# Kernel optimization log

Hardware: AMD Instinct MI355X
Metric: run time of the kernel (lower is better)

The kernel has to match this reference:

```python
import jax, jax.numpy as jnp
import numpy as np

N = 50000
E = 800000
NODE_DIM = 128
EDGE_DIM = 32
HIDDEN = 128


def _linear_params(key, fan_in, fan_out):
    kw, kb = jax.random.split(key)
    bound = 1.0 / np.sqrt(fan_in)
    W = jax.random.uniform(kw, (fan_in, fan_out), minval=-bound, maxval=bound, dtype=jnp.float32)
    b = jax.random.uniform(kb, (fan_out,), minval=-bound, maxval=bound, dtype=jnp.float32)
    return W, b


def setup_inputs() -> dict:
    key = jax.random.key(0)
    ks = jax.random.split(key, 7)
    h = jax.random.normal(ks[0], (N, NODE_DIM), dtype=jnp.float32)
    edge_index = jax.random.randint(ks[1], (2, E), 0, N, dtype=jnp.int64)
    edge_attr = jax.random.normal(ks[2], (E, EDGE_DIM), dtype=jnp.float32)
    # message_fn: Linear(2*node+edge -> hidden), ReLU, Linear(hidden -> hidden), ReLU
    Wm1, bm1 = _linear_params(ks[3], 2 * NODE_DIM + EDGE_DIM, HIDDEN)
    Wm2, bm2 = _linear_params(ks[4], HIDDEN, HIDDEN)
    # update_fn: Linear(node+hidden -> hidden), ReLU, Linear(hidden -> node)
    Wu1, bu1 = _linear_params(ks[5], NODE_DIM + HIDDEN, HIDDEN)
    Wu2, bu2 = _linear_params(ks[6], HIDDEN, NODE_DIM)
    return {"h": h, "edge_attr": edge_attr, "Wm1": Wm1, "bm1": bm1, "Wm2": Wm2, "bm2": bm2,
            "Wu1": Wu1, "bu1": bu1, "Wu2": Wu2, "bu2": bu2, "edge_index": edge_index}


def reference(h, edge_attr, Wm1, bm1, Wm2, bm2, Wu1, bu1, Wu2, bu2, edge_index):
    src = edge_index[0]
    dst = edge_index[1]
    # m_ij = phi_m(h_i, h_j, e_ij)
    msg_input = jnp.concatenate([h[src], h[dst], edge_attr], axis=-1)  # (E, 2*node+edge)
    x = jax.nn.relu(msg_input @ Wm1 + bm1)
    messages = jax.nn.relu(x @ Wm2 + bm2)  # (E, hidden)
    # scatter-add over destination nodes
    agg = jax.ops.segment_sum(messages, dst, num_segments=N)  # (N, hidden)
    # h_i' = h_i + phi_u(h_i, agg_i)
    update_input = jnp.concatenate([h, agg], axis=-1)
    u = jax.nn.relu(update_input @ Wu1 + bu1)
    h_new = h + (u @ Wu2 + bu2)
    return h_new
```

## Files before the change

### kernel.cpp

```cpp
#include <hip/hip_runtime.h>

#define NN 50000
#define NE 800000

typedef __attribute__((ext_vector_type(8))) short bf16x8;
typedef __attribute__((ext_vector_type(4))) float f32x4;

__device__ __forceinline__ short f2bf(float f) {
    union { float f; unsigned u; } v; v.f = f;
    return (short)((v.u + 0x7fffu + ((v.u >> 16) & 1u)) >> 16);
}

__device__ __forceinline__ float bf2f(short s) {
    union { unsigned u; float f; } v;
    v.u = ((unsigned)(unsigned short)s) << 16;
    return v.f;
}

__device__ __forceinline__ bf16x8 cvt8(const float* __restrict__ p) {
    const f32x4 a = *(const f32x4*)p;
    const f32x4 b = *(const f32x4*)(p + 4);
    bf16x8 r;
#pragma unroll
    for (int j = 0; j < 4; ++j) { r[j] = f2bf(a[j]); r[j + 4] = f2bf(b[j]); }
    return r;
}

__device__ __forceinline__ void gld_lds16(const short* g, short* l) {
    __builtin_amdgcn_global_load_lds(
        (const __attribute__((address_space(1))) void*)g,
        (__attribute__((address_space(3))) void*)l, 16, 0, 0);
}

#define GW_M1A 0
#define GW_M1B 16384
#define GW_1C  32768
#define GW_M2S 36864
#define GW_U1A 53248
#define GW_U1B 69632
#define GW_U2S 86016
#define GW_TOT 102400

template<int KROWS, int NTHREADS>
__device__ __forceinline__ void stage_w(const float* __restrict__ W, short* lds, int tid) {
    constexpr int NSLOT = (KROWS / 32) * 8 * 64;
#pragma unroll 1
    for (int slot = tid; slot < NSLOT; slot += NTHREADS) {
        const int f = slot >> 6, l = slot & 63;
        const int s = f >> 3, t = f & 7;
        const int k0 = 32 * s + ((l >> 4) << 3);
        const int n = 16 * t + (l & 15);
        bf16x8 v;
#pragma unroll
        for (int j = 0; j < 8; ++j) v[j] = f2bf(W[(k0 + j) * 128 + n]);
        *(bf16x8*)(lds + slot * 8) = v;
    }
}

template<int NSLOT, int NTHREADS>
__device__ __forceinline__ void stage_copy(const short* __restrict__ g, short* lds, int tid) {
#pragma unroll 1
    for (int s = tid; s < NSLOT; s += NTHREADS) {
        *(bf16x8*)(lds + (size_t)s * 8) = *(const bf16x8*)(g + (size_t)s * 8);
    }
}


__global__ __launch_bounds__(256) void mega_kernel(
    const float* __restrict__ h, const float* __restrict__ Wm1,
    const float* __restrict__ bm1, const float* __restrict__ Wm2,
    const float* __restrict__ Wu1, const float* __restrict__ Wu2,
    const int* __restrict__ eidx, short* __restrict__ gW,
    short* __restrict__ Pb, short* __restrict__ Qb, int* __restrict__ cnt)
{
    const int b = blockIdx.x;
    const int tid = threadIdx.x;
    if (b < 512) {
        __shared__ short sWa[16384];
        __shared__ short sWb[16384];
        stage_w<128, 256>(Wm1, sWa, tid);
        stage_w<128, 256>(Wm1 + 128 * 128, sWb, tid);
        __syncthreads();
        const int wave = tid >> 6, lane = tid & 63;
        const int q = lane >> 4, col = lane & 15;
        float b1v[8];
#pragma unroll
        for (int t = 0; t < 8; ++t) b1v[t] = bm1[t * 16 + col];
        for (int tile = b * 4 + wave; tile < NN / 16; tile += 2048) {
            const int r0 = tile * 16;
            f32x4 aP[8], aQ[8];
#pragma unroll
            for (int t = 0; t < 8; ++t) {
                aP[t] = {0.f, 0.f, 0.f, 0.f};
                const float bb = b1v[t];
                aQ[t] = {bb, bb, bb, bb};
            }
#pragma unroll
            for (int s = 0; s < 4; ++s) {
                const bf16x8 ah = cvt8(&h[(r0 + col) * 128 + s * 32 + q * 8]);
#pragma unroll
                for (int t = 0; t < 8; ++t) {
                    const bf16x8 ba = *(const bf16x8*)(sWa + ((s * 8 + t) * 64 + lane) * 8);
                    const bf16x8 bb = *(const bf16x8*)(sWb + ((s * 8 + t) * 64 + lane) * 8);
                    aP[t] = __builtin_amdgcn_mfma_f32_16x16x32_bf16(ah, ba, aP[t], 0, 0, 0);
                    aQ[t] = __builtin_amdgcn_mfma_f32_16x16x32_bf16(ah, bb, aQ[t], 0, 0, 0);
                }
            }
#pragma unroll
            for (int r = 0; r < 4; ++r) {
                const size_t row = (size_t)(r0 + q * 4 + r) * 128;
                bf16x8 vp, vq;
#pragma unroll
                for (int t = 0; t < 8; ++t) { vp[t] = f2bf(aP[t][r]); vq[t] = f2bf(aQ[t][r]); }
                *(bf16x8*)(Pb + row + col * 8) = vp;
                *(bf16x8*)(Qb + row + col * 8) = vq;
            }
        }
    } else if (b < 562) {
        const int slot = (b - 512) * 256 + tid;
        if (slot < 12800) {
            const float* W; int local; bool sigma = false;
            if (slot < 2048)       { W = Wm1;             local = slot; }
            else if (slot < 4096)  { W = Wm1 + 128 * 128; local = slot - 2048; }
            else if (slot < 4608)  { W = Wm1 + 256 * 128; local = slot - 4096; }
            else if (slot < 6656)  { W = Wm2;             local = slot - 4608; sigma = true; }
            else if (slot < 8704)  { W = Wu1;             local = slot - 6656; }
            else if (slot < 10752) { W = Wu1 + 128 * 128; local = slot - 8704; }
            else                   { W = Wu2;             local = slot - 10752; sigma = true; }
            const int f = local >> 6, l = local & 63;
            const int s = f >> 3, t = f & 7;
            const int k0 = 32 * s + ((l >> 4) << 3);
            const int n = 16 * t + (l & 15);
            bf16x8 v;
#pragma unroll
            for (int j = 0; j < 8; ++j) {
                int k = k0 + j;
                if (sigma) k = (k & 7) * 16 + (k >> 3);
                v[j] = f2bf(W[k * 128 + n]);
            }
            *(bf16x8*)(gW + (size_t)slot * 8) = v;
        }
    } else {
        const int e = (b - 562) * 256 + tid;
        if (e < NE) atomicAdd(&cnt[eidx[NE + e]], 1);
    }
}


__global__ __launch_bounds__(1024) void scan1_kernel(const int* __restrict__ cnt,
                                                     int* __restrict__ part,
                                                     int* __restrict__ bsum) {
    __shared__ int s[1024];
    const int t = threadIdx.x;
    const int i = blockIdx.x * 1024 + t;
    const int v = (i < NN) ? cnt[i] : 0;
    int x = v;
    s[t] = x;
    __syncthreads();
    for (int off = 1; off < 1024; off <<= 1) {
        const int y = (t >= off) ? s[t - off] : 0;
        __syncthreads();
        x += y;
        s[t] = x;
        __syncthreads();
    }
    if (i < NN) part[i] = x - v;
    if (t == 1023) bsum[blockIdx.x] = x;
}

__global__ __launch_bounds__(1024) void scan23_kernel(const int* __restrict__ part,
                                                      const int* __restrict__ bsum,
                                                      int* __restrict__ cursor) {
    __shared__ int off;
    if (threadIdx.x == 0) {
        int a = 0;
        for (int bb = 0; bb < (int)blockIdx.x; ++bb) a += bsum[bb];
        off = a;
    }
    __syncthreads();
    const int i = blockIdx.x * 1024 + threadIdx.x;
    if (i < NN) cursor[i] = part[i] + off;
}


__global__ void scatter_kernel(const int* __restrict__ eidx, int* __restrict__ cursor,
                               const float* __restrict__ ea,
                               int2* __restrict__ sd2, short* __restrict__ eb) {
    const int e = blockIdx.x * blockDim.x + threadIdx.x;
    if (e < NE) {
        const int d = eidx[NE + e];
        const int pos = atomicAdd(&cursor[d], 1);
        sd2[pos] = make_int2(eidx[e], d);
        const float* src = ea + (size_t)e * 32;
        short* dst = eb + (size_t)pos * 32;
#pragma unroll
        for (int j = 0; j < 4; ++j) {
            const f32x4 a = *(const f32x4*)(src + j * 8);
            const f32x4 bq = *(const f32x4*)(src + j * 8 + 4);
            bf16x8 v;
#pragma unroll
            for (int k = 0; k < 4; ++k) { v[k] = f2bf(a[k]); v[4 + k] = f2bf(bq[k]); }
            *(bf16x8*)(dst + j * 8) = v;
        }
    }
}

#define WPB 7
#define TPW 28

__global__ __launch_bounds__(448, 2) void edge_kernel(
    const short* __restrict__ Pb, const short* __restrict__ Qb,
    const short* __restrict__ eb, const short* __restrict__ gW,
    const float* __restrict__ bm2,
    const int2* __restrict__ sd2, float* __restrict__ agg)
{
    __shared__ short sW2[16384];
    __shared__ short sW1c[4096];
    __shared__ short sPool[WPB][2][4096];
    const int tid = threadIdx.x;
    const int wave = tid >> 6, lane = tid & 63;
    const int q = lane >> 4, col = lane & 15;
    const int NT = NE / 16;
    float b2v[8];
#pragma unroll
    for (int t = 0; t < 8; ++t) b2v[t] = bm2[t * 16 + col];
    stage_copy<2048, 448>(gW + GW_M2S, sW2, tid);
    stage_copy<512, 448>(gW + GW_1C, sW1c, tid);

    const int wg = blockIdx.x * WPB + wave;
    const int t_begin = wg * TPW;
    const int t_end = (t_begin + TPW < NT) ? (t_begin + TPW) : NT;
    const bool act = t_begin < t_end;

    short* bufc = &sPool[wave][0][0];
    short* bufa = &sPool[wave][1][0];
    int2 sd_c[4], sd_n[4];
    bf16x8 aea_c;

    if (act) {
        {
            const int e0 = t_begin * 16;
            const int4 a0 = *(const int4*)(sd2 + e0 + q * 4);
            const int4 a1 = *(const int4*)(sd2 + e0 + q * 4 + 2);
            sd_c[0] = make_int2(a0.x, a0.y); sd_c[1] = make_int2(a0.z, a0.w);
            sd_c[2] = make_int2(a1.x, a1.y); sd_c[3] = make_int2(a1.z, a1.w);
        }
#pragma unroll
        for (int r = 0; r < 4; ++r) {
            gld_lds16(Pb + (size_t)sd_c[r].x * 128 + col * 8, bufc + r * 512);
            gld_lds16(Qb + (size_t)sd_c[r].y * 128 + col * 8, bufc + 2048 + r * 512);
        }
        {
            const int t1 = (t_begin + 1 < t_end) ? t_begin + 1 : t_begin;
            const int e1 = t1 * 16;
            const int4 a0 = *(const int4*)(sd2 + e1 + q * 4);
            const int4 a1 = *(const int4*)(sd2 + e1 + q * 4 + 2);
            sd_n[0] = make_int2(a0.x, a0.y); sd_n[1] = make_int2(a0.z, a0.w);
            sd_n[2] = make_int2(a1.x, a1.y); sd_n[3] = make_int2(a1.z, a1.w);
        }
        aea_c = *(const bf16x8*)(eb + (size_t)(t_begin * 16 + col) * 32 + q * 8);
    }
    __syncthreads();

    for (int tile = t_begin; tile < t_end; ++tile) {
        const int tn = (tile + 1 < t_end) ? tile + 1 : tile;
        asm volatile("s_waitcnt vmcnt(0)" ::: "memory");
        bf16x8 vp[4], vq[4];
#pragma unroll
        for (int r = 0; r < 4; ++r) {
            vp[r] = *(const bf16x8*)(bufc + r * 512 + lane * 8);
            vq[r] = *(const bf16x8*)(bufc + 2048 + r * 512 + lane * 8);
        }
#pragma unroll
        for (int r = 0; r < 4; ++r) {
            gld_lds16(Pb + (size_t)sd_n[r].x * 128 + col * 8, bufa + r * 512);
            gld_lds16(Qb + (size_t)sd_n[r].y * 128 + col * 8, bufa + 2048 + r * 512);
        }
        const bf16x8 aea_n = *(const bf16x8*)(eb + (size_t)(tn * 16 + col) * 32 + q * 8);
        int2 sd_n2[4];
        {
            const int t2 = (tile + 2 < t_end) ? tile + 2 : t_end - 1;
            const int e2 = t2 * 16;
            const int4 a0 = *(const int4*)(sd2 + e2 + q * 4);
            const int4 a1 = *(const int4*)(sd2 + e2 + q * 4 + 2);
            sd_n2[0] = make_int2(a0.x, a0.y); sd_n2[1] = make_int2(a0.z, a0.w);
            sd_n2[2] = make_int2(a1.x, a1.y); sd_n2[3] = make_int2(a1.z, a1.w);
        }
        const int prev3 = __shfl_up(sd_c[3].y, 16);
        unsigned qm = 0;
        if (q > 0 && sd_c[0].y == prev3) qm |= 1u;
        if (sd_c[1].y == sd_c[0].y) qm |= 2u;
        if (sd_c[2].y == sd_c[1].y) qm |= 4u;
        if (sd_c[3].y == sd_c[2].y) qm |= 8u;
        const unsigned o1 = (unsigned)__shfl_xor((int)qm, 16);
        const unsigned o2 = (unsigned)__shfl_xor((int)qm, 32);
        const unsigned o3 = (unsigned)__shfl_xor((int)o1, 32);
        const unsigned eqmask = (qm << (q * 4)) | (o1 << ((q ^ 1) * 4)) |
                                (o2 << ((q ^ 2) * 4)) | (o3 << ((q ^ 3) * 4));
        f32x4 acc1[8];
#pragma unroll
        for (int r = 0; r < 4; ++r) {
            const bf16x8 vpr = vp[r], vqr = vq[r];
#pragma unroll
            for (int t = 0; t < 8; ++t)
                acc1[t][r] = bf2f(vpr[t]) + bf2f(vqr[t]);
        }
#pragma unroll
        for (int t = 0; t < 8; ++t) {
            const bf16x8 bw = *(const bf16x8*)(sW1c + (t * 64 + lane) * 8);
            acc1[t] = __builtin_amdgcn_mfma_f32_16x16x32_bf16(aea_c, bw, acc1[t], 0, 0, 0);
        }
        short* myX = bufc;
#pragma unroll
        for (int r = 0; r < 4; ++r) {
            bf16x8 vx;
#pragma unroll
            for (int t = 0; t < 8; ++t) {
                const float x = acc1[t][r];
                vx[t] = f2bf(x > 0.f ? x : 0.f);
            }
            *(bf16x8*)(myX + (q * 4 + r) * 136 + col * 8) = vx;
        }
        f32x4 acc2[8];
#pragma unroll
        for (int t = 0; t < 8; ++t) {
            const float b = b2v[t];
            acc2[t] = {b, b, b, b};
        }
#pragma unroll
        for (int s = 0; s < 4; ++s) {
            const bf16x8 ax = *(const bf16x8*)(myX + col * 136 + s * 32 + q * 8);
#pragma unroll
            for (int t = 0; t < 8; ++t) {
                const bf16x8 bw = *(const bf16x8*)(sW2 + ((s * 8 + t) * 64 + lane) * 8);
                acc2[t] = __builtin_amdgcn_mfma_f32_16x16x32_bf16(ax, bw, acc2[t], 0, 0, 0);
            }
        }
        if (eqmask == 0xFFFEu) {
#pragma unroll
            for (int t = 0; t < 8; ++t) {
                float m0 = acc2[t][0]; m0 = m0 > 0.f ? m0 : 0.f;
                float m1 = acc2[t][1]; m1 = m1 > 0.f ? m1 : 0.f;
                float m2 = acc2[t][2]; m2 = m2 > 0.f ? m2 : 0.f;
                float m3 = acc2[t][3]; m3 = m3 > 0.f ? m3 : 0.f;
                float s = (m0 + m1) + (m2 + m3);
                s += __shfl_xor(s, 16);
                s += __shfl_xor(s, 32);
                if (q == 0 && s != 0.f)
                    unsafeAtomicAdd(&agg[(size_t)sd_c[0].y * 128 + t * 16 + col], s);
            }
        } else {
            int head[4], qe[4];
#pragma unroll
            for (int r = 0; r < 4; ++r) {
                const int e = q * 4 + r;
                head[r] = !((eqmask >> e) & 1u);
                const unsigned after = ~(eqmask >> (e + 1));
                const int run = __builtin_ctz(after);
                qe[r] = (e + run) >> 2;
            }
#pragma unroll
            for (int t = 0; t < 8; ++t) {
                float m0 = acc2[t][0]; m0 = m0 > 0.f ? m0 : 0.f;
                float m1 = acc2[t][1]; m1 = m1 > 0.f ? m1 : 0.f;
                float m2 = acc2[t][2]; m2 = m2 > 0.f ? m2 : 0.f;
                float m3 = acc2[t][3]; m3 = m3 > 0.f ? m3 : 0.f;
                const float s3 = m3;
                const float s2 = m2 + ((qm & 8u) ? s3 : 0.f);
                const float s1 = m1 + ((qm & 4u) ? s2 : 0.f);
                const float s0 = m0 + ((qm & 2u) ? s1 : 0.f);
                const float p1 = __shfl_xor(s0, 16);
                const float p2 = __shfl_xor(s0, 32);
                const float p3 = __shfl_xor(p1, 32);
                const float seg[4] = {s0, s1, s2, s3};
#pragma unroll
                for (int r = 0; r < 4; ++r) {
                    if (head[r]) {
                        float tot = seg[r];
#pragma unroll
                        for (int j = 1; j < 4; ++j) {
                            if (j > q && j <= qe[r]) {
                                const int jx = j ^ q;
                                tot += (jx == 1) ? p1 : (jx == 2) ? p2 : p3;
                            }
                        }
                        if (tot != 0.f)
                            unsafeAtomicAdd(&agg[(size_t)sd_c[r].y * 128 + t * 16 + col], tot);
                    }
                }
            }
        }
#pragma unroll
        for (int r = 0; r < 4; ++r) { sd_c[r] = sd_n[r]; sd_n[r] = sd_n2[r]; }
        aea_c = aea_n;
        short* tmp = bufc; bufc = bufa; bufa = tmp;
    }
}


__global__ __launch_bounds__(512) void update_kernel(
    const float* __restrict__ h, const float* __restrict__ agg,
    const short* __restrict__ gW, const float* __restrict__ bu1,
    const float* __restrict__ bu2, float* __restrict__ out)
{
    __shared__ short sWa[16384];
    __shared__ short sWb[16384];
    __shared__ short sW2[16384];
    __shared__ short sX[8][16 * 136];
    const int tid = threadIdx.x;
    const int wave = tid >> 6, lane = tid & 63;
    const int q = lane >> 4, col = lane & 15;
    float b1v[8], b2v[8];
#pragma unroll
    for (int t = 0; t < 8; ++t) { b1v[t] = bu1[t * 16 + col]; b2v[t] = bu2[t * 16 + col]; }
    stage_copy<2048, 512>(gW + GW_U1A, sWa, tid);
    stage_copy<2048, 512>(gW + GW_U1B, sWb, tid);
    stage_copy<2048, 512>(gW + GW_U2S, sW2, tid);
    __syncthreads();
    short* myX = &sX[wave][0];
    for (int tile = blockIdx.x * 8 + wave; tile < NN / 16; tile += gridDim.x * 8) {
        const int r0 = tile * 16;
        f32x4 acc1[8];
#pragma unroll
        for (int t = 0; t < 8; ++t) {
            const float b = b1v[t];
            acc1[t] = {b, b, b, b};
        }
#pragma unroll
        for (int s = 0; s < 4; ++s) {
            const bf16x8 ahh = cvt8(&h[(r0 + col) * 128 + s * 32 + q * 8]);
            const bf16x8 aag = cvt8(&agg[(r0 + col) * 128 + s * 32 + q * 8]);
#pragma unroll
            for (int t = 0; t < 8; ++t) {
                const bf16x8 ba = *(const bf16x8*)(sWa + ((s * 8 + t) * 64 + lane) * 8);
                const bf16x8 bb = *(const bf16x8*)(sWb + ((s * 8 + t) * 64 + lane) * 8);
                acc1[t] = __builtin_amdgcn_mfma_f32_16x16x32_bf16(ahh, ba, acc1[t], 0, 0, 0);
                acc1[t] = __builtin_amdgcn_mfma_f32_16x16x32_bf16(aag, bb, acc1[t], 0, 0, 0);
            }
        }
#pragma unroll
        for (int r = 0; r < 4; ++r) {
            bf16x8 vx;
#pragma unroll
            for (int t = 0; t < 8; ++t) {
                const float x = acc1[t][r];
                vx[t] = f2bf(x > 0.f ? x : 0.f);
            }
            *(bf16x8*)(myX + (q * 4 + r) * 136 + col * 8) = vx;
        }
        f32x4 acc2[8];
#pragma unroll
        for (int t = 0; t < 8; ++t) {
            const float b = b2v[t];
#pragma unroll
            for (int r = 0; r < 4; ++r)
                acc2[t][r] = b + h[(r0 + q * 4 + r) * 128 + t * 16 + col];
        }
#pragma unroll
        for (int s = 0; s < 4; ++s) {
            const bf16x8 ax = *(const bf16x8*)(myX + col * 136 + s * 32 + q * 8);
#pragma unroll
            for (int t = 0; t < 8; ++t) {
                const bf16x8 bw = *(const bf16x8*)(sW2 + ((s * 8 + t) * 64 + lane) * 8);
                acc2[t] = __builtin_amdgcn_mfma_f32_16x16x32_bf16(ax, bw, acc2[t], 0, 0, 0);
            }
        }
#pragma unroll
        for (int t = 0; t < 8; ++t)
#pragma unroll
            for (int r = 0; r < 4; ++r)
                out[(r0 + q * 4 + r) * 128 + t * 16 + col] = acc2[t][r];
    }
}

extern "C" void kernel_launch(void* const* d_in, const int* in_sizes, int n_in,
                              void* d_out, int out_size, void* d_ws, size_t ws_size,
                              hipStream_t stream) {
    const float* h   = (const float*)d_in[0];
    const float* ea  = (const float*)d_in[1];
    const float* Wm1 = (const float*)d_in[2];
    const float* bm1 = (const float*)d_in[3];
    const float* Wm2 = (const float*)d_in[4];
    const float* bm2 = (const float*)d_in[5];
    const float* Wu1 = (const float*)d_in[6];
    const float* bu1 = (const float*)d_in[7];
    const float* Wu2 = (const float*)d_in[8];
    const float* bu2 = (const float*)d_in[9];
    const int* eidx  = (const int*)d_in[10];
    float* out = (float*)d_out;

    short* gW  = (short*)d_ws;
    short* Pb  = gW + GW_TOT;
    short* Qb  = Pb + (size_t)NN * 128;
    float* agg = (float*)(Qb + (size_t)NN * 128);
    int* cnt    = (int*)(agg + (size_t)NN * 128);
    int* part   = cnt + NN;
    int* bsum   = part + NN;
    int* cursor = bsum + 64;
    int2* sd2   = (int2*)(cursor + NN);
    short* eb   = (short*)(sd2 + NE);

    const int NB_SCAN = (NN + 1023) / 1024;
    const int NB_E = (NE + 255) / 256;

    hipMemsetAsync(cnt, 0, (size_t)NN * sizeof(int), stream);
    hipMemsetAsync(agg, 0, (size_t)NN * 128 * sizeof(float), stream);
    mega_kernel<<<512 + 50 + NB_E, 256, 0, stream>>>(h, Wm1, bm1, Wm2, Wu1, Wu2,
                                                     eidx, gW, Pb, Qb, cnt);
    scan1_kernel<<<NB_SCAN, 1024, 0, stream>>>(cnt, part, bsum);
    scan23_kernel<<<NB_SCAN, 1024, 0, stream>>>(part, bsum, cursor);
    scatter_kernel<<<NB_E, 256, 0, stream>>>(eidx, cursor, ea, sd2, eb);
    edge_kernel<<<256, 448, 0, stream>>>(Pb, Qb, eb, gW, bm2, sd2, agg);
    update_kernel<<<256, 512, 0, stream>>>(h, agg, gW, bu1, bu2, out);
}
```

Baseline: 570.3 us.

## Use packed bf16 converts, hoist edge-tile LDS reads, stream update weights from global

Replaces the scalar float-to-bf16 rounding with the hardware v_cvt_pk_bf16_f32 instruction in every kernel, so conversion costs fewer ALU instructions. The edge kernel now reads the next tile's gathered P/Q rows from LDS after the second GEMM rather than at the top of the loop, hiding the wait on the async loads, and its launch bound is relaxed to one block per CU for more registers. The update kernel stages only one weight matrix in LDS, reads the other two straight from global memory, and launches twice as many blocks to raise occupancy. The risk is higher global and cache traffic for those weight reads, and possible occupancy loss in the edge kernel.

```diff
diff --git a/kernel.cpp b/kernel.cpp
--- a/kernel.cpp
+++ b/kernel.cpp
@@ -17,13 +17,21 @@
     return v.f;
 }
 
+__device__ __forceinline__ unsigned cvtpk(float lo, float hi) {
+    unsigned r;
+    asm("v_cvt_pk_bf16_f32 %0, %1, %2" : "=v"(r) : "v"(lo), "v"(hi));
+    return r;
+}
+
+union bf8u { unsigned u[4]; bf16x8 v; };
+
 __device__ __forceinline__ bf16x8 cvt8(const float* __restrict__ p) {
     const f32x4 a = *(const f32x4*)p;
     const f32x4 b = *(const f32x4*)(p + 4);
-    bf16x8 r;
-#pragma unroll
-    for (int j = 0; j < 4; ++j) { r[j] = f2bf(a[j]); r[j + 4] = f2bf(b[j]); }
-    return r;
+    bf8u r;
+    r.u[0] = cvtpk(a[0], a[1]); r.u[1] = cvtpk(a[2], a[3]);
+    r.u[2] = cvtpk(b[0], b[1]); r.u[3] = cvtpk(b[2], b[3]);
+    return r.v;
 }
 
 __device__ __forceinline__ void gld_lds16(const short* g, short* l) {
@@ -50,10 +58,13 @@
         const int s = f >> 3, t = f & 7;
         const int k0 = 32 * s + ((l >> 4) << 3);
         const int n = 16 * t + (l & 15);
-        bf16x8 v;
-#pragma unroll
-        for (int j = 0; j < 8; ++j) v[j] = f2bf(W[(k0 + j) * 128 + n]);
-        *(bf16x8*)(lds + slot * 8) = v;
+        float w[8];
+#pragma unroll
+        for (int j = 0; j < 8; ++j) w[j] = W[(k0 + j) * 128 + n];
+        bf8u v;
+#pragma unroll
+        for (int j = 0; j < 4; ++j) v.u[j] = cvtpk(w[2 * j], w[2 * j + 1]);
+        *(bf16x8*)(lds + slot * 8) = v.v;
     }
 }
 
@@ -109,11 +120,14 @@
 #pragma unroll
             for (int r = 0; r < 4; ++r) {
                 const size_t row = (size_t)(r0 + q * 4 + r) * 128;
-                bf16x8 vp, vq;
-#pragma unroll
-                for (int t = 0; t < 8; ++t) { vp[t] = f2bf(aP[t][r]); vq[t] = f2bf(aQ[t][r]); }
-                *(bf16x8*)(Pb + row + col * 8) = vp;
-                *(bf16x8*)(Qb + row + col * 8) = vq;
+                bf8u vp, vq;
+#pragma unroll
+                for (int j = 0; j < 4; ++j) {
+                    vp.u[j] = cvtpk(aP[2 * j][r], aP[2 * j + 1][r]);
+                    vq.u[j] = cvtpk(aQ[2 * j][r], aQ[2 * j + 1][r]);
+                }
+                *(bf16x8*)(Pb + row + col * 8) = vp.v;
+                *(bf16x8*)(Qb + row + col * 8) = vq.v;
             }
         }
     } else if (b < 562) {
@@ -131,14 +145,17 @@
             const int s = f >> 3, t = f & 7;
             const int k0 = 32 * s + ((l >> 4) << 3);
             const int n = 16 * t + (l & 15);
-            bf16x8 v;
+            float w[8];
 #pragma unroll
             for (int j = 0; j < 8; ++j) {
                 int k = k0 + j;
                 if (sigma) k = (k & 7) * 16 + (k >> 3);
-                v[j] = f2bf(W[k * 128 + n]);
-            }
-            *(bf16x8*)(gW + (size_t)slot * 8) = v;
+                w[j] = W[k * 128 + n];
+            }
+            bf8u v;
+#pragma unroll
+            for (int j = 0; j < 4; ++j) v.u[j] = cvtpk(w[2 * j], w[2 * j + 1]);
+            *(bf16x8*)(gW + (size_t)slot * 8) = v.v;
         }
     } else {
         const int e = (b - 562) * 256 + tid;
@@ -197,10 +214,10 @@
         for (int j = 0; j < 4; ++j) {
             const f32x4 a = *(const f32x4*)(src + j * 8);
             const f32x4 bq = *(const f32x4*)(src + j * 8 + 4);
-            bf16x8 v;
-#pragma unroll
-            for (int k = 0; k < 4; ++k) { v[k] = f2bf(a[k]); v[4 + k] = f2bf(bq[k]); }
-            *(bf16x8*)(dst + j * 8) = v;
+            bf8u v;
+            v.u[0] = cvtpk(a[0], a[1]);  v.u[1] = cvtpk(a[2], a[3]);
+            v.u[2] = cvtpk(bq[0], bq[1]); v.u[3] = cvtpk(bq[2], bq[3]);
+            *(bf16x8*)(dst + j * 8) = v.v;
         }
     }
 }
@@ -208,7 +225,7 @@
 #define WPB 7
 #define TPW 28
 
-__global__ __launch_bounds__(448, 2) void edge_kernel(
+__global__ __launch_bounds__(448, 1) void edge_kernel(
     const short* __restrict__ Pb, const short* __restrict__ Qb,
     const short* __restrict__ eb, const short* __restrict__ gW,
     const float* __restrict__ bm2,
@@ -236,6 +253,7 @@
     short* bufa = &sPool[wave][1][0];
     int2 sd_c[4], sd_n[4];
     bf16x8 aea_c;
+    bf16x8 vp[4], vq[4];
 
     if (act) {
         {
@@ -261,16 +279,17 @@
         aea_c = *(const bf16x8*)(eb + (size_t)(t_begin * 16 + col) * 32 + q * 8);
     }
     __syncthreads();
+    if (act) {
+        asm volatile("s_waitcnt vmcnt(0)" ::: "memory");
+#pragma unroll
+        for (int r = 0; r < 4; ++r) {
+            vp[r] = *(const bf16x8*)(bufc + r * 512 + lane * 8);
+            vq[r] = *(const bf16x8*)(bufc + 2048 + r * 512 + lane * 8);
+        }
+    }
 
     for (int tile = t_begin; tile < t_end; ++tile) {
         const int tn = (tile + 1 < t_end) ? tile + 1 : tile;
-        asm volatile("s_waitcnt vmcnt(0)" ::: "memory");
-        bf16x8 vp[4], vq[4];
-#pragma unroll
-        for (int r = 0; r < 4; ++r) {
-            vp[r] = *(const bf16x8*)(bufc + r * 512 + lane * 8);
-            vq[r] = *(const bf16x8*)(bufc + 2048 + r * 512 + lane * 8);
-        }
 #pragma unroll
         for (int r = 0; r < 4; ++r) {
             gld_lds16(Pb + (size_t)sd_n[r].x * 128 + col * 8, bufa + r * 512);
@@ -313,13 +332,13 @@
         short* myX = bufc;
 #pragma unroll
         for (int r = 0; r < 4; ++r) {
-            bf16x8 vx;
-#pragma unroll
-            for (int t = 0; t < 8; ++t) {
-                const float x = acc1[t][r];
-                vx[t] = f2bf(x > 0.f ? x : 0.f);
-            }
-            *(bf16x8*)(myX + (q * 4 + r) * 136 + col * 8) = vx;
+            float m[8];
+#pragma unroll
+            for (int t = 0; t < 8; ++t) { const float x = acc1[t][r]; m[t] = x > 0.f ? x : 0.f; }
+            bf8u vx;
+#pragma unroll
+            for (int j = 0; j < 4; ++j) vx.u[j] = cvtpk(m[2 * j], m[2 * j + 1]);
+            *(bf16x8*)(myX + (q * 4 + r) * 136 + col * 8) = vx.v;
         }
         f32x4 acc2[8];
 #pragma unroll
@@ -335,6 +354,12 @@
                 const bf16x8 bw = *(const bf16x8*)(sW2 + ((s * 8 + t) * 64 + lane) * 8);
                 acc2[t] = __builtin_amdgcn_mfma_f32_16x16x32_bf16(ax, bw, acc2[t], 0, 0, 0);
             }
+        }
+        asm volatile("s_waitcnt vmcnt(0)" ::: "memory");
+#pragma unroll
+        for (int r = 0; r < 4; ++r) {
+            vp[r] = *(const bf16x8*)(bufa + r * 512 + lane * 8);
+            vq[r] = *(const bf16x8*)(bufa + 2048 + r * 512 + lane * 8);
         }
         if (eqmask == 0xFFFEu) {
 #pragma unroll
@@ -404,8 +429,6 @@
     const float* __restrict__ bu2, float* __restrict__ out)
 {
     __shared__ short sWa[16384];
-    __shared__ short sWb[16384];
-    __shared__ short sW2[16384];
     __shared__ short sX[8][16 * 136];
     const int tid = threadIdx.x;
     const int wave = tid >> 6, lane = tid & 63;
@@ -414,9 +437,9 @@
 #pragma unroll
     for (int t = 0; t < 8; ++t) { b1v[t] = bu1[t * 16 + col]; b2v[t] = bu2[t * 16 + col]; }
     stage_copy<2048, 512>(gW + GW_U1A, sWa, tid);
-    stage_copy<2048, 512>(gW + GW_U1B, sWb, tid);
-    stage_copy<2048, 512>(gW + GW_U2S, sW2, tid);
     __syncthreads();
+    const short* gWb = gW + GW_U1B;
+    const short* gW2 = gW + GW_U2S;
     short* myX = &sX[wave][0];
     for (int tile = blockIdx.x * 8 + wave; tile < NN / 16; tile += gridDim.x * 8) {
         const int r0 = tile * 16;
@@ -433,20 +456,20 @@
 #pragma unroll
             for (int t = 0; t < 8; ++t) {
                 const bf16x8 ba = *(const bf16x8*)(sWa + ((s * 8 + t) * 64 + lane) * 8);
-                const bf16x8 bb = *(const bf16x8*)(sWb + ((s * 8 + t) * 64 + lane) * 8);
+                const bf16x8 bb = *(const bf16x8*)(gWb + ((s * 8 + t) * 64 + lane) * 8);
                 acc1[t] = __builtin_amdgcn_mfma_f32_16x16x32_bf16(ahh, ba, acc1[t], 0, 0, 0);
                 acc1[t] = __builtin_amdgcn_mfma_f32_16x16x32_bf16(aag, bb, acc1[t], 0, 0, 0);
             }
         }
 #pragma unroll
         for (int r = 0; r < 4; ++r) {
-            bf16x8 vx;
-#pragma unroll
-            for (int t = 0; t < 8; ++t) {
-                const float x = acc1[t][r];
-                vx[t] = f2bf(x > 0.f ? x : 0.f);
-            }
-            *(bf16x8*)(myX + (q * 4 + r) * 136 + col * 8) = vx;
+            float m[8];
+#pragma unroll
+            for (int t = 0; t < 8; ++t) { const float x = acc1[t][r]; m[t] = x > 0.f ? x : 0.f; }
+            bf8u vx;
+#pragma unroll
+            for (int j = 0; j < 4; ++j) vx.u[j] = cvtpk(m[2 * j], m[2 * j + 1]);
+            *(bf16x8*)(myX + (q * 4 + r) * 136 + col * 8) = vx.v;
         }
         f32x4 acc2[8];
 #pragma unroll
@@ -461,7 +484,7 @@
             const bf16x8 ax = *(const bf16x8*)(myX + col * 136 + s * 32 + q * 8);
 #pragma unroll
             for (int t = 0; t < 8; ++t) {
-                const bf16x8 bw = *(const bf16x8*)(sW2 + ((s * 8 + t) * 64 + lane) * 8);
+                const bf16x8 bw = *(const bf16x8*)(gW2 + ((s * 8 + t) * 64 + lane) * 8);
                 acc2[t] = __builtin_amdgcn_mfma_f32_16x16x32_bf16(ax, bw, acc2[t], 0, 0, 0);
             }
         }
@@ -511,5 +534,5 @@
     scan23_kernel<<<NB_SCAN, 1024, 0, stream>>>(part, bsum, cursor);
     scatter_kernel<<<NB_E, 256, 0, stream>>>(eidx, cursor, ea, sd2, eb);
     edge_kernel<<<256, 448, 0, stream>>>(Pb, Qb, eb, gW, bm2, sd2, agg);
-    update_kernel<<<256, 512, 0, stream>>>(h, agg, gW, bu1, bu2, out);
-}
+    update_kernel<<<512, 512, 0, stream>>>(h, agg, gW, bu1, bu2, out);
+}
```

Measured after the change: 461.7 us. 19.0% less time.
